# Optimization experiments

Hardware: AMD Instinct MI355X
Metric: run time of the kernel (lower is better)

## Reference

```python
import jax, jax.numpy as jnp
import numpy as np

B, N, DIN, DOUT = 8, 2048, 512, 512

def setup_inputs() -> dict:
    key = jax.random.key(0)
    kx, ka, kw, kb, kattn = jax.random.split(key, 5)
    x = jax.random.normal(kx, (B, N, DIN), dtype=jnp.float32)
    adjacency_matrix = jax.random.randint(ka, (B, N, N), 0, 2, dtype=jnp.int32)
    # nn.Linear(in,out): weight [out,in], bias [out]
    lim_w = float(np.sqrt(1.0 / DIN))
    W = jax.random.uniform(kw, (DOUT, DIN), minval=-lim_w, maxval=lim_w, dtype=jnp.float32)
    b = jax.random.uniform(kb, (DOUT,), minval=-lim_w, maxval=lim_w, dtype=jnp.float32)
    # xavier_uniform for attn [out,out]
    lim_a = float(np.sqrt(6.0 / (DOUT + DOUT)))
    attn = jax.random.uniform(kattn, (DOUT, DOUT), minval=-lim_a, maxval=lim_a, dtype=jnp.float32)
    return {"x": x, "adjacency_matrix": adjacency_matrix, "W": W, "b": b, "attn": attn}

def reference(x, adjacency_matrix, W, b, attn):
    h = jnp.einsum('bni,oi->bno', x, W) + b                 # [B,N,DOUT]
    ha = jnp.einsum('bmi,ij->bmj', h, attn)                  # h @ attn
    scores = jnp.einsum('bmj,bnj->bmn', ha, h)               # bilinear pairwise scores
    scores = jnp.where(adjacency_matrix == 0, -jnp.inf, scores)
    attn_weights = jax.nn.softmax(scores, axis=-1)           # adjacency-masked softmax
    x_out = jnp.einsum('bmn,bnd->bmd', attn_weights, h)      # weighted aggregation
    return jax.nn.elu(x_out)
```

## Files before the change

### kernel.cpp

```cpp
#include <hip/hip_runtime.h>
#include <cstdint>
#include <cstddef>

typedef unsigned short u16;
using f16x8 = __attribute__((ext_vector_type(8))) _Float16;
using f32x4 = __attribute__((ext_vector_type(4))) float;
using u16x4 = __attribute__((ext_vector_type(4))) unsigned short;

__device__ __forceinline__ u16 f2h(float f) {
  union { _Float16 h; u16 u; } c;
  c.h = (_Float16)f;
  return c.u;
}

__device__ __forceinline__ void gl_lds16(const void* g, void* lds) {
  __builtin_amdgcn_global_load_lds(
      (const __attribute__((address_space(1))) void*)(uintptr_t)g,
      (__attribute__((address_space(3))) void*)(uint32_t)(uintptr_t)lds,
      16, 0, 0);
}

template <int MODE>
__global__ __launch_bounds__(256) void gemm_bt(
    const u16* __restrict__ A, const u16* __restrict__ Bt,
    void* __restrict__ Cv, const float* __restrict__ bias,
    int M, int Ncols, int K,
    long long strideA, long long strideB, long long strideC)
{
  __shared__ __align__(16) u16 sA[128 * 32];
  __shared__ __align__(16) u16 sB[128 * 32];

  const int bz = blockIdx.z;
  A  += (size_t)bz * strideA;
  Bt += (size_t)bz * strideB;

  const int m0 = blockIdx.y * 128;
  const int n0 = blockIdx.x * 128;
  const int t    = threadIdx.x;
  const int lane = t & 63;
  const int wave = t >> 6;
  const int wm   = (wave >> 1) * 64;
  const int wn   = (wave & 1) * 64;
  const int lm   = lane & 15;
  const int quad = lane >> 4;

  f32x4 acc[4][4];
#pragma unroll
  for (int i = 0; i < 4; ++i)
#pragma unroll
    for (int j = 0; j < 4; ++j) acc[i][j] = f32x4{0.f, 0.f, 0.f, 0.f};

  const int r0 = t >> 2,        c0 = t & 3;
  const int r1 = (t + 256) >> 2, c1 = t & 3;
  const int ldsb0 = (t & ~63) * 8;
  const int ldsb1 = ((t & ~63) + 256) * 8;

  const int nk = K >> 5;
  for (int kc = 0; kc < nk; ++kc) {
    const int kb = kc * 32;
    gl_lds16(A  + (size_t)(m0 + r0) * K + kb + c0 * 8, sA + ldsb0);
    gl_lds16(A  + (size_t)(m0 + r1) * K + kb + c1 * 8, sA + ldsb1);
    gl_lds16(Bt + (size_t)(n0 + r0) * K + kb + c0 * 8, sB + ldsb0);
    gl_lds16(Bt + (size_t)(n0 + r1) * K + kb + c1 * 8, sB + ldsb1);
    __syncthreads();

    f16x8 af[4], bf[4];
#pragma unroll
    for (int i = 0; i < 4; ++i) {
      af[i] = *(const f16x8*)(sA + (wm + i * 16 + lm) * 32 + quad * 8);
      bf[i] = *(const f16x8*)(sB + (wn + i * 16 + lm) * 32 + quad * 8);
    }
#pragma unroll
    for (int i = 0; i < 4; ++i)
#pragma unroll
      for (int j = 0; j < 4; ++j)
        acc[i][j] = __builtin_amdgcn_mfma_f32_16x16x32_f16(af[i], bf[j], acc[i][j], 0, 0, 0);
    __syncthreads();
  }

  if (MODE == 0) {
    u16* C = (u16*)Cv + (size_t)bz * strideC;
#pragma unroll
    for (int j = 0; j < 4; ++j) {
      const int col = n0 + wn + j * 16 + lm;
      const float bv = bias ? bias[col] : 0.f;
#pragma unroll
      for (int i = 0; i < 4; ++i)
#pragma unroll
        for (int r = 0; r < 4; ++r) {
          const int row = m0 + wm + i * 16 + quad * 4 + r;
          C[(size_t)row * Ncols + col] = f2h(acc[i][j][r] + bv);
        }
    }
  } else {
    float* C = (float*)Cv + (size_t)bz * strideC;
#pragma unroll
    for (int j = 0; j < 4; ++j) {
      const int col = n0 + wn + j * 16 + lm;
#pragma unroll
      for (int i = 0; i < 4; ++i)
#pragma unroll
        for (int r = 0; r < 4; ++r) {
          const int row = m0 + wm + i * 16 + quad * 4 + r;
          float v = acc[i][j][r];
          if (MODE == 2) v = v > 0.f ? v : expm1f(v);
          C[(size_t)row * Ncols + col] = v;
        }
    }
  }
}

__global__ __launch_bounds__(256) void masked_softmax(
    const float* __restrict__ S, const int* __restrict__ adj, u16* __restrict__ P)
{
  const size_t row = blockIdx.x;
  const float* s = S + row * 2048;
  const int*   a = adj + row * 2048;
  u16*         p = P + row * 2048;
  const int t = threadIdx.x;

  float v[8];
#pragma unroll
  for (int i = 0; i < 2; ++i) {
    float4 sv = ((const float4*)s)[t + i * 256];
    int4   av = ((const int4*)a)[t + i * 256];
    v[i * 4 + 0] = av.x ? sv.x : -1e30f;
    v[i * 4 + 1] = av.y ? sv.y : -1e30f;
    v[i * 4 + 2] = av.z ? sv.z : -1e30f;
    v[i * 4 + 3] = av.w ? sv.w : -1e30f;
  }
  float mx = v[0];
#pragma unroll
  for (int i = 1; i < 8; ++i) mx = fmaxf(mx, v[i]);
#pragma unroll
  for (int o = 32; o > 0; o >>= 1) mx = fmaxf(mx, __shfl_xor(mx, o));
  __shared__ float red[4];
  if ((t & 63) == 0) red[t >> 6] = mx;
  __syncthreads();
  mx = fmaxf(fmaxf(red[0], red[1]), fmaxf(red[2], red[3]));
  __syncthreads();

  float e[8]; float sum = 0.f;
#pragma unroll
  for (int i = 0; i < 8; ++i) { e[i] = __expf(v[i] - mx); sum += e[i]; }
#pragma unroll
  for (int o = 32; o > 0; o >>= 1) sum += __shfl_xor(sum, o);
  if ((t & 63) == 0) red[t >> 6] = sum;
  __syncthreads();
  sum = red[0] + red[1] + red[2] + red[3];
  const float inv = 1.f / sum;

#pragma unroll
  for (int i = 0; i < 2; ++i) {
    u16x4 o4;
    o4[0] = f2h(e[i * 4 + 0] * inv);
    o4[1] = f2h(e[i * 4 + 1] * inv);
    o4[2] = f2h(e[i * 4 + 2] * inv);
    o4[3] = f2h(e[i * 4 + 3] * inv);
    ((u16x4*)p)[t + i * 256] = o4;
  }
}

__global__ __launch_bounds__(256) void transpose_u16(
    const u16* __restrict__ in, u16* __restrict__ outp, int R, int C)
{
  __shared__ u16 tile[64][65];
  const size_t base = (size_t)blockIdx.z * R * C;
  const int r0 = blockIdx.y * 64, c0 = blockIdx.x * 64;
  const int t = threadIdx.x;
  const int c = t & 63, rr = t >> 6;
#pragma unroll
  for (int i = 0; i < 16; ++i) {
    const int r = rr + i * 4;
    tile[r][c] = in[base + (size_t)(r0 + r) * C + c0 + c];
  }
  __syncthreads();
  const int rp = t & 63, cc = t >> 6;
#pragma unroll
  for (int i = 0; i < 16; ++i) {
    const int cq = cc + i * 4;
    outp[base + (size_t)(c0 + cq) * R + r0 + rp] = tile[rp][cq];
  }
}

__global__ __launch_bounds__(256) void cvt_f32_f16(
    const float* __restrict__ in, u16* __restrict__ outp, int n4)
{
  const int i = blockIdx.x * 256 + threadIdx.x;
  if (i >= n4) return;
  float4 v = ((const float4*)in)[i];
  u16x4 o; o[0] = f2h(v.x); o[1] = f2h(v.y); o[2] = f2h(v.z); o[3] = f2h(v.w);
  ((u16x4*)outp)[i] = o;
}

__global__ __launch_bounds__(256) void transpose_cvt(
    const float* __restrict__ in, u16* __restrict__ outp, int R, int C)
{
  const int idx = blockIdx.x * 256 + threadIdx.x;
  const int i = idx / C, j = idx % C;
  outp[(size_t)j * R + i] = f2h(in[idx]);
}

extern "C" void kernel_launch(void* const* d_in, const int* in_sizes, int n_in,
                              void* d_out, int out_size, void* d_ws, size_t ws_size,
                              hipStream_t stream) {
  (void)in_sizes; (void)n_in; (void)out_size;
  const float* x    = (const float*)d_in[0];
  const int*   adj  = (const int*)d_in[1];
  const float* W    = (const float*)d_in[2];
  const float* bvec = (const float*)d_in[3];
  const float* attn = (const float*)d_in[4];
  float* out = (float*)d_out;

  constexpr int B = 8, N = 2048, D = 512;
  constexpr size_t MN = (size_t)B * N;

  char* ws = (char*)d_ws;
  size_t off = 0;
  auto take = [&](size_t bytes) -> char* {
    char* p = ws + off;
    off += (bytes + 255) & ~(size_t)255;
    return p;
  };
  u16* xh   = (u16*)take(MN * D * 2);
  u16* Wh   = (u16*)take((size_t)D * D * 2);
  u16* attT = (u16*)take((size_t)D * D * 2);
  u16* h    = (u16*)take(MN * D * 2);
  u16* hT   = (u16*)take(MN * D * 2);
  u16* ha   = (u16*)take(MN * D * 2);

  auto al = [](size_t b) { return (b + 255) & ~(size_t)255; };
  const size_t szSf = al((size_t)B * N * N * 4), szPf = al((size_t)B * N * N * 2);
  const size_t szSb = al((size_t)N * N * 4),     szPb = al((size_t)N * N * 2);
  const bool full  = ws_size >= off + szSf + szPf;
  const bool ok_pb = ws_size >= off + szSb + szPb;
  if (!full && !ok_pb) return;

  cvt_f32_f16<<<dim3((unsigned)(MN * D / 4 / 256)), 256, 0, stream>>>(x, xh, (int)(MN * D / 4));
  cvt_f32_f16<<<dim3(D * D / 4 / 256), 256, 0, stream>>>(W, Wh, D * D / 4);
  transpose_cvt<<<dim3(D * D / 256), 256, 0, stream>>>(attn, attT, D, D);

  gemm_bt<0><<<dim3(D / 128, MN / 128, 1), 256, 0, stream>>>(
      xh, Wh, h, bvec, (int)MN, D, D, 0, 0, 0);
  transpose_u16<<<dim3(D / 64, N / 64, B), 256, 0, stream>>>(h, hT, N, D);
  gemm_bt<0><<<dim3(D / 128, MN / 128, 1), 256, 0, stream>>>(
      h, attT, ha, nullptr, (int)MN, D, D, 0, 0, 0);

  if (full) {
    float* S = (float*)take(szSf);
    u16*   P = (u16*)take(szPf);
    gemm_bt<1><<<dim3(N / 128, N / 128, B), 256, 0, stream>>>(
        ha, h, S, nullptr, N, N, D,
        (long long)N * D, (long long)N * D, (long long)N * N);
    masked_softmax<<<dim3((unsigned)(B * N)), 256, 0, stream>>>(S, adj, P);
    gemm_bt<2><<<dim3(D / 128, N / 128, B), 256, 0, stream>>>(
        P, hT, out, nullptr, N, D, N,
        (long long)N * N, (long long)D * N, (long long)N * D);
  } else {
    float* S = (float*)take(szSb);
    u16*   P = (u16*)take(szPb);
    for (int b = 0; b < B; ++b) {
      gemm_bt<1><<<dim3(N / 128, N / 128, 1), 256, 0, stream>>>(
          ha + (size_t)b * N * D, h + (size_t)b * N * D, S, nullptr, N, N, D, 0, 0, 0);
      masked_softmax<<<dim3(N), 256, 0, stream>>>(S, adj + (size_t)b * N * N, P);
      gemm_bt<2><<<dim3(D / 128, N / 128, 1), 256, 0, stream>>>(
          P, hT + (size_t)b * D * N, out + (size_t)b * N * D, nullptr, N, D, N, 0, 0, 0);
    }
  }
}
```

Measured before the change: 452.1 us.

## Replace 128x128 GEMM with double-buffered 256-row tiles and BK=64

Replaces the 128x128, K=32 single-buffered GEMM with a 512-thread kernel using 256-row tiles (128 or 256 columns), K-step 64, and double-buffered LDS staging via global_load_lds. The next K tile is prefetched while MFMAs run on the current one, and one barrier per iteration is dropped. Larger tiles raise operand reuse per LDS byte. The trade-off is much larger LDS use (up to 128 KB), which limits occupancy to one block per CU, and fewer blocks for the smaller GEMMs. The loads are issued into the alternate buffer with no explicit vmcnt wait before the barrier, so correctness relies on the compiler inserting the wait.

```diff
diff --git a/kernel.cpp b/kernel.cpp
--- a/kernel.cpp
+++ b/kernel.cpp
@@ -20,89 +20,109 @@
       16, 0, 0);
 }
 
-template <int MODE>
-__global__ __launch_bounds__(256) void gemm_bt(
+template <int ROWS>
+__device__ __forceinline__ void stage_tile(const u16* g, int ldk, u16* lds, int t) {
+#pragma unroll
+  for (int i = 0; i < ROWS / 64; ++i) {
+    const int s = i * 512 + t;
+    gl_lds16(g + (size_t)(s >> 3) * ldk + (s & 7) * 8,
+             lds + (size_t)(i * 512 + (t & ~63)) * 8);
+  }
+}
+
+template <int BN, int MODE>
+__global__ __launch_bounds__(512) void gemm256(
     const u16* __restrict__ A, const u16* __restrict__ Bt,
     void* __restrict__ Cv, const float* __restrict__ bias,
     int M, int Ncols, int K,
     long long strideA, long long strideB, long long strideC)
 {
-  __shared__ __align__(16) u16 sA[128 * 32];
-  __shared__ __align__(16) u16 sB[128 * 32];
+  constexpr int NF = BN / 64;
+  __shared__ __align__(16) u16 sA[2][256 * 64];
+  __shared__ __align__(16) u16 sB[2][BN * 64];
 
   const int bz = blockIdx.z;
   A  += (size_t)bz * strideA;
   Bt += (size_t)bz * strideB;
 
-  const int m0 = blockIdx.y * 128;
-  const int n0 = blockIdx.x * 128;
+  const int m0 = blockIdx.y * 256;
+  const int n0 = blockIdx.x * BN;
   const int t    = threadIdx.x;
   const int lane = t & 63;
   const int wave = t >> 6;
-  const int wm   = (wave >> 1) * 64;
-  const int wn   = (wave & 1) * 64;
+  const int wm   = (wave >> 2) * 128;
+  const int wn   = (wave & 3) * (BN / 4);
   const int lm   = lane & 15;
   const int quad = lane >> 4;
 
-  f32x4 acc[4][4];
-#pragma unroll
-  for (int i = 0; i < 4; ++i)
-#pragma unroll
-    for (int j = 0; j < 4; ++j) acc[i][j] = f32x4{0.f, 0.f, 0.f, 0.f};
-
-  const int r0 = t >> 2,        c0 = t & 3;
-  const int r1 = (t + 256) >> 2, c1 = t & 3;
-  const int ldsb0 = (t & ~63) * 8;
-  const int ldsb1 = ((t & ~63) + 256) * 8;
-
-  const int nk = K >> 5;
-  for (int kc = 0; kc < nk; ++kc) {
-    const int kb = kc * 32;
-    gl_lds16(A  + (size_t)(m0 + r0) * K + kb + c0 * 8, sA + ldsb0);
-    gl_lds16(A  + (size_t)(m0 + r1) * K + kb + c1 * 8, sA + ldsb1);
-    gl_lds16(Bt + (size_t)(n0 + r0) * K + kb + c0 * 8, sB + ldsb0);
-    gl_lds16(Bt + (size_t)(n0 + r1) * K + kb + c1 * 8, sB + ldsb1);
-    __syncthreads();
-
-    f16x8 af[4], bf[4];
-#pragma unroll
-    for (int i = 0; i < 4; ++i) {
-      af[i] = *(const f16x8*)(sA + (wm + i * 16 + lm) * 32 + quad * 8);
-      bf[i] = *(const f16x8*)(sB + (wn + i * 16 + lm) * 32 + quad * 8);
-    }
-#pragma unroll
-    for (int i = 0; i < 4; ++i)
-#pragma unroll
-      for (int j = 0; j < 4; ++j)
-        acc[i][j] = __builtin_amdgcn_mfma_f32_16x16x32_f16(af[i], bf[j], acc[i][j], 0, 0, 0);
-    __syncthreads();
+  f32x4 acc[8][NF];
+#pragma unroll
+  for (int i = 0; i < 8; ++i)
+#pragma unroll
+    for (int j = 0; j < NF; ++j) acc[i][j] = f32x4{0.f, 0.f, 0.f, 0.f};
+
+  const u16* Ag = A + (size_t)m0 * K;
+  const u16* Bg = Bt + (size_t)n0 * K;
+
+  const int nk = K >> 6;
+  stage_tile<256>(Ag, K, sA[0], t);
+  stage_tile<BN >(Bg, K, sB[0], t);
+  __syncthreads();
+
+  for (int kt = 0; kt < nk; ++kt) {
+    const int cur = kt & 1;
+    if (kt + 1 < nk) {
+      stage_tile<256>(Ag + ((kt + 1) << 6), K, sA[cur ^ 1], t);
+      stage_tile<BN >(Bg + ((kt + 1) << 6), K, sB[cur ^ 1], t);
+    }
+
+    const u16* pA = sA[cur];
+    const u16* pB = sB[cur];
+    f16x8 bf[NF][2];
+#pragma unroll
+    for (int nf = 0; nf < NF; ++nf)
+#pragma unroll
+      for (int ks = 0; ks < 2; ++ks)
+        bf[nf][ks] = *(const f16x8*)(pB + (wn + nf * 16 + lm) * 64 + ks * 32 + quad * 8);
+#pragma unroll
+    for (int mf = 0; mf < 8; ++mf) {
+      const u16* ra = pA + (wm + mf * 16 + lm) * 64 + quad * 8;
+      f16x8 a0 = *(const f16x8*)(ra);
+      f16x8 a1 = *(const f16x8*)(ra + 32);
+#pragma unroll
+      for (int nf = 0; nf < NF; ++nf) {
+        acc[mf][nf] = __builtin_amdgcn_mfma_f32_16x16x32_f16(a0, bf[nf][0], acc[mf][nf], 0, 0, 0);
+        acc[mf][nf] = __builtin_amdgcn_mfma_f32_16x16x32_f16(a1, bf[nf][1], acc[mf][nf], 0, 0, 0);
+      }
+    }
+    if (kt + 1 < nk) __syncthreads();
   }
 
   if (MODE == 0) {
     u16* C = (u16*)Cv + (size_t)bz * strideC;
 #pragma unroll
-    for (int j = 0; j < 4; ++j) {
-      const int col = n0 + wn + j * 16 + lm;
+    for (int nf = 0; nf < NF; ++nf) {
+      const int col = n0 + wn + nf * 16 + lm;
       const float bv = bias ? bias[col] : 0.f;
 #pragma unroll
-      for (int i = 0; i < 4; ++i)
+      for (int mf = 0; mf < 8; ++mf)
 #pragma unroll
         for (int r = 0; r < 4; ++r) {
-          const int row = m0 + wm + i * 16 + quad * 4 + r;
-          C[(size_t)row * Ncols + col] = f2h(acc[i][j][r] + bv);
+          const int row = m0 + wm + mf * 16 + quad * 4 + r;
+          C[(size_t)row * Ncols + col] = f2h(acc[mf][nf][r] + bv);
         }
     }
   } else {
     float* C = (float*)Cv + (size_t)bz * strideC;
 #pragma unroll
-    for (int j = 0; j < 4; ++j) {
-      const int col = n0 + wn + j * 16 + lm;
-#pragma unroll
-      for (int i = 0; i < 4; ++i)
+    for (int nf = 0; nf < NF; ++nf) {
+      const int col = n0 + wn + nf * 16 + lm;
+#pragma unroll
+      for (int mf = 0; mf < 8; ++mf)
 #pragma unroll
         for (int r = 0; r < 4; ++r) {
-          const int row = m0 + wm + i * 16 + quad * 4 + r;
-          float v = acc[i][j][r];
+          const int row = m0 + wm + mf * 16 + quad * 4 + r;
+          float v = acc[mf][nf][r];
           if (MODE == 2) v = v > 0.f ? v : expm1f(v);
           C[(size_t)row * Ncols + col] = v;
         }
@@ -240,30 +260,30 @@
   cvt_f32_f16<<<dim3(D * D / 4 / 256), 256, 0, stream>>>(W, Wh, D * D / 4);
   transpose_cvt<<<dim3(D * D / 256), 256, 0, stream>>>(attn, attT, D, D);
 
-  gemm_bt<0><<<dim3(D / 128, MN / 128, 1), 256, 0, stream>>>(
+  gemm256<128, 0><<<dim3(D / 128, MN / 256, 1), 512, 0, stream>>>(
       xh, Wh, h, bvec, (int)MN, D, D, 0, 0, 0);
   transpose_u16<<<dim3(D / 64, N / 64, B), 256, 0, stream>>>(h, hT, N, D);
-  gemm_bt<0><<<dim3(D / 128, MN / 128, 1), 256, 0, stream>>>(
+  gemm256<128, 0><<<dim3(D / 128, MN / 256, 1), 512, 0, stream>>>(
       h, attT, ha, nullptr, (int)MN, D, D, 0, 0, 0);
 
   if (full) {
     float* S = (float*)take(szSf);
     u16*   P = (u16*)take(szPf);
-    gemm_bt<1><<<dim3(N / 128, N / 128, B), 256, 0, stream>>>(
+    gemm256<256, 1><<<dim3(N / 256, N / 256, B), 512, 0, stream>>>(
         ha, h, S, nullptr, N, N, D,
         (long long)N * D, (long long)N * D, (long long)N * N);
     masked_softmax<<<dim3((unsigned)(B * N)), 256, 0, stream>>>(S, adj, P);
-    gemm_bt<2><<<dim3(D / 128, N / 128, B), 256, 0, stream>>>(
+    gemm256<128, 2><<<dim3(D / 128, N / 256, B), 512, 0, stream>>>(
         P, hT, out, nullptr, N, D, N,
         (long long)N * N, (long long)D * N, (long long)N * D);
   } else {
     float* S = (float*)take(szSb);
     u16*   P = (u16*)take(szPb);
     for (int b = 0; b < B; ++b) {
-      gemm_bt<1><<<dim3(N / 128, N / 128, 1), 256, 0, stream>>>(
+      gemm256<256, 1><<<dim3(N / 256, N / 256, 1), 512, 0, stream>>>(
           ha + (size_t)b * N * D, h + (size_t)b * N * D, S, nullptr, N, N, D, 0, 0, 0);
       masked_softmax<<<dim3(N), 256, 0, stream>>>(S, adj + (size_t)b * N * N, P);
-      gemm_bt<2><<<dim3(D / 128, N / 128, 1), 256, 0, stream>>>(
+      gemm256<128, 2><<<dim3(D / 128, N / 256, 1), 512, 0, stream>>>(
           P, hT + (size_t)b * D * N, out + (size_t)b * N * D, nullptr, N, D, N, 0, 0, 0);
     }
   }
```

After: 432.2 us. -4.4%, faster.
